# Kernel tuning notes

Measured on AMD Instinct MI355X. Metric: run time of the kernel, lower is better.

The kernel has to match this reference:

```python
import jax, jax.numpy as jnp
import numpy as np

B, K, D, R, NH, NN = 1024, 20, 128, 3, 2, 100000
DM = 3 * D          # d_model = node + edge + time feat concat
DK = DM // NH       # per-head dim
NEG = -1e10


def setup_inputs():
    key = jax.random.key(0)
    ks = jax.random.split(key, 24)
    node_table = jax.random.normal(ks[0], (NN, D), jnp.float32)
    node_table = node_table.at[0].set(0.0)  # padding_idx=0
    s = 1.0 / np.sqrt(DM)
    return {
        'src_idx': jax.random.randint(ks[1], (B,), 0, NN),
        'cut_time': jax.random.uniform(ks[2], (B,), jnp.float32) * 100.0,
        'ngh1_nodes': jax.random.randint(ks[3], (B, K), 0, NN),
        'ngh1_t': jax.random.uniform(ks[4], (B, K), jnp.float32) * 100.0,
        'ngh1_rel': jax.random.uniform(ks[5], (B, K, R), jnp.float32),
        'ngh2_nodes': jax.random.randint(ks[6], (B * K, K), 0, NN),
        'ngh2_t': jax.random.uniform(ks[7], (B * K, K), jnp.float32) * 100.0,
        'ngh2_rel': jax.random.uniform(ks[8], (B * K, K, R), jnp.float32),
        'node_table': node_table,
        'basis_freq': jnp.asarray(1.0 / np.power(10.0, np.linspace(0, 9, D)), jnp.float32),
        'phase': jnp.zeros((D,), jnp.float32),
        'rel_W': jax.random.normal(ks[9], (R, D), jnp.float32) * 0.1,
        'rel_b': jnp.zeros((D,), jnp.float32),
        'w_q': jax.random.normal(ks[10], (2, DM, DM), jnp.float32) * s,
        'w_k': jax.random.normal(ks[11], (2, DM, DM), jnp.float32) * s,
        'w_v': jax.random.normal(ks[12], (2, DM, DM), jnp.float32) * s,
        'fc_W': jax.random.normal(ks[13], (2, DM, DM), jnp.float32) * s,
        'fc_b': jnp.zeros((2, DM), jnp.float32),
        'ln_g': jnp.ones((2, DM), jnp.float32),
        'ln_b': jnp.zeros((2, DM), jnp.float32),
        'mg1_W': jax.random.normal(ks[14], (2, DM + D, D), jnp.float32) * 0.05,
        'mg1_b': jnp.zeros((2, D), jnp.float32),
        'mg2_W': jax.random.normal(ks[15], (2, D, D), jnp.float32) * 0.09,
        'mg2_b': jnp.zeros((2, D), jnp.float32),
    }


def _layer_norm(x, g, b, eps=1e-5):
    mu = x.mean(axis=-1, keepdims=True)
    var = ((x - mu) ** 2).mean(axis=-1, keepdims=True)
    return (x - mu) / jnp.sqrt(var + eps) * g + b


def _attn_agg(src, src_t, seq, seq_t, seq_e, mask,
              wq, wk, wv, fcW, fcb, g, b, m1W, m1b, m2W, m2b):
    # src [Bb,D], src_t [Bb,1,D], seq/seq_t/seq_e [Bb,N,D], mask [Bb,N] (True = pad)
    Bb, N = seq.shape[0], seq.shape[1]
    src_ext = src[:, None, :]
    q = jnp.concatenate([src_ext, jnp.zeros_like(src_ext), src_t], axis=2)  # [Bb,1,3D]
    k = jnp.concatenate([seq, seq_e, seq_t], axis=2)                        # [Bb,N,3D]
    qh = (q @ wq).reshape(Bb, 1, NH, DK)
    kh = (k @ wk).reshape(Bb, N, NH, DK)
    vh = (k @ wv).reshape(Bb, N, NH, DK)
    sc = jnp.einsum('bqhd,bkhd->bhqk', qh, kh) / jnp.sqrt(jnp.float32(DK))
    sc = jnp.where(mask[:, None, None, :], NEG, sc)
    attn = jax.nn.softmax(sc, axis=-1)
    out = jnp.einsum('bhqk,bkhd->bqhd', attn, vh).reshape(Bb, 1, DM)
    out = _layer_norm(out @ fcW + fcb + q, g, b)[:, 0]  # residual + LN, squeeze q-len
    h = jax.nn.relu(jnp.concatenate([out, src], axis=1) @ m1W + m1b)  # MergeLayer
    return h @ m2W + m2b


def reference(src_idx, cut_time, ngh1_nodes, ngh1_t, ngh1_rel,
              ngh2_nodes, ngh2_t, ngh2_rel,
              node_table, basis_freq, phase, rel_W, rel_b,
              w_q, w_k, w_v, fc_W, fc_b, ln_g, ln_b,
              mg1_W, mg1_b, mg2_W, mg2_b):
    def tenc(ts):  # TimeEncode: cos(t*w + phi), ts [..., L] -> [..., L, D]
        return jnp.cos(ts[..., None] * basis_freq + phase)

    def layer(l, src, src_t, seq, seq_t, seq_e, mask):
        return _attn_agg(src, src_t, seq, seq_t, seq_e, mask,
                         w_q[l], w_k[l], w_v[l], fc_W[l], fc_b[l],
                         ln_g[l], ln_b[l], mg1_W[l], mg1_b[l], mg2_W[l], mg2_b[l])

    feat_src = node_table[src_idx]              # [B,D]  (layer-0 conv feat)
    feat_n1 = node_table[ngh1_nodes]            # [B,K,D]
    feat_n2 = node_table[ngh2_nodes]            # [B*K,K,D]
    zt_src = tenc(jnp.zeros((B, 1), jnp.float32))      # time embed of 0 for queries
    zt_n1 = tenc(jnp.zeros((B * K, 1), jnp.float32))
    t1e = tenc(cut_time[:, None] - ngh1_t)              # [B,K,D]
    t2e = tenc(ngh1_t.reshape(-1)[:, None] - ngh2_t)    # [B*K,K,D]
    r1 = ngh1_rel @ rel_W + rel_b               # MultiHotLayer relation embed
    r2 = ngh2_rel @ rel_W + rel_b
    m1 = ngh1_nodes == 0
    m2 = ngh2_nodes == 0

    # layer 1 (attn_model_list[0]) applied to src and to flattened 1-hop neighbors
    src_l1 = layer(0, feat_src, zt_src, feat_n1, t1e, r1, m1)                      # [B,D]
    n1_l1 = layer(0, feat_n1.reshape(B * K, D), zt_n1, feat_n2, t2e, r2, m2)       # [B*K,D]
    # layer 2 (attn_model_list[1])
    out = layer(1, src_l1, zt_src, n1_l1.reshape(B, K, D), t1e, r1, m1)            # [B,D]
    return out
```

## Files before the change

### kernel.cpp

```cpp
#include <hip/hip_runtime.h>

typedef unsigned int u32;
typedef unsigned short u16;

typedef short bf16x8 __attribute__((ext_vector_type(8)));
typedef float f32x4 __attribute__((ext_vector_type(4)));

#define DD 128
#define DMM 384
#define KNB 20

__device__ __forceinline__ u16 f2b(float f){
  u32 u = __float_as_uint(f);
  u += 0x7fffu + ((u >> 16) & 1u);
  return (u16)(u >> 16);
}
__device__ __forceinline__ float b2f(u32 h){ return __uint_as_float(h << 16); }

__global__ void zt_kernel(const float* __restrict__ phase, float* __restrict__ zt){
  int d = threadIdx.x;
  if (d < DD) zt[d] = cosf(phase[d]);
}

__global__ void tcvt_kernel(const float* __restrict__ src, u16* __restrict__ dst, int K, int N){
  int i = blockIdx.x * 256 + threadIdx.x;
  if (i >= K * N) return;
  int k = i / N, n = i - k * N;
  dst[(size_t)n * K + k] = f2b(src[i]);
}

__global__ __launch_bounds__(256) void build_k_kernel(
  const float* __restrict__ node_table,
  const int*   __restrict__ nodes,
  const float* __restrict__ feat_override,
  const float* __restrict__ t_src,
  const float* __restrict__ t_ngh,
  const float* __restrict__ rel,
  const float* __restrict__ relW, const float* __restrict__ relb,
  const float* __restrict__ bfreq, const float* __restrict__ phase,
  u16* __restrict__ kmat, int nrows)
{
  int lr = blockIdx.x * 2 + (threadIdx.x >> 7);
  if (lr >= nrows) return;
  int d = threadIdx.x & 127;
  int b = lr / KNB;
  float f;
  if (feat_override) f = feat_override[(size_t)lr * DD + d];
  else { int nd = nodes[lr]; f = node_table[(size_t)nd * DD + d]; }
  float r0 = rel[(size_t)lr * 3 + 0], r1 = rel[(size_t)lr * 3 + 1], r2 = rel[(size_t)lr * 3 + 2];
  float re = r0 * relW[d] + r1 * relW[DD + d] + r2 * relW[2 * DD + d] + relb[d];
  float dt = t_src[b] - t_ngh[lr];
  float te = cosf(dt * bfreq[d] + phase[d]);
  u16* kr = kmat + (size_t)lr * DMM;
  kr[d] = f2b(f); kr[DD + d] = f2b(re); kr[2 * DD + d] = f2b(te);
}

__global__ __launch_bounds__(256) void build_q_kernel(
  const float* __restrict__ node_table,
  const int*   __restrict__ src_nodes,
  const float* __restrict__ feat_override,
  const float* __restrict__ zt,
  u16* __restrict__ qmat, float* __restrict__ srcf,
  int nb)
{
  int r = blockIdx.x * 2 + (threadIdx.x >> 7);
  if (r >= nb) return;
  int d = threadIdx.x & 127;
  float s = feat_override ? feat_override[(size_t)r * DD + d]
                          : node_table[(size_t)src_nodes[r] * DD + d];
  size_t q0 = (size_t)r * DMM;
  qmat[q0 + d] = f2b(s); qmat[q0 + DD + d] = 0; qmat[q0 + 2 * DD + d] = f2b(zt[d]);
  srcf[(size_t)r * DD + d] = s;
}

#define SAS 40
__global__ __launch_bounds__(256) void gemm_kernel(
  const u16* __restrict__ A, const u16* __restrict__ BT,
  const float* __restrict__ bias,
  float* __restrict__ Cf, u16* __restrict__ Cb,
  int M, int N, int K, int relu)
{
  __shared__ __align__(16) u16 lds[2 * 128 * SAS];
  u16* As = lds; u16* Bs = lds + 128 * SAS;
  int tid = threadIdx.x;
  int lane = tid & 63, w = tid >> 6;
  int wm = w >> 1, wn = w & 1;
  int bm = blockIdx.x, bn = blockIdx.y;
  f32x4 acc[4][4] = {};
  int r0 = tid >> 2;
  int c0 = tid & 3;
  const u16* Abase = A + (size_t)(bm * 128) * K;
  const u16* Bbase = BT + (size_t)(bn * 128) * K;
  int rr = lane & 15, kq = lane >> 4;
  for (int kt = 0; kt < K; kt += 32) {
    uint4 a0 = *(const uint4*)(Abase + (size_t)r0 * K + kt + c0 * 8);
    uint4 a1 = *(const uint4*)(Abase + (size_t)(r0 + 64) * K + kt + c0 * 8);
    uint4 b0 = *(const uint4*)(Bbase + (size_t)r0 * K + kt + c0 * 8);
    uint4 b1 = *(const uint4*)(Bbase + (size_t)(r0 + 64) * K + kt + c0 * 8);
    __syncthreads();
    *(uint4*)&As[r0 * SAS + c0 * 8] = a0;
    *(uint4*)&As[(r0 + 64) * SAS + c0 * 8] = a1;
    *(uint4*)&Bs[r0 * SAS + c0 * 8] = b0;
    *(uint4*)&Bs[(r0 + 64) * SAS + c0 * 8] = b1;
    __syncthreads();
    bf16x8 af[4], bf[4];
    #pragma unroll
    for (int i = 0; i < 4; i++) af[i] = *(const bf16x8*)&As[(wm * 64 + i * 16 + rr) * SAS + kq * 8];
    #pragma unroll
    for (int j = 0; j < 4; j++) bf[j] = *(const bf16x8*)&Bs[(wn * 64 + j * 16 + rr) * SAS + kq * 8];
    #pragma unroll
    for (int i = 0; i < 4; i++)
      #pragma unroll
      for (int j = 0; j < 4; j++)
        acc[i][j] = __builtin_amdgcn_mfma_f32_16x16x32_bf16(af[i], bf[j], acc[i][j], 0, 0, 0);
  }
  int drow = lane >> 4, dcol = lane & 15;
  #pragma unroll
  for (int i = 0; i < 4; i++) {
    #pragma unroll
    for (int j = 0; j < 4; j++) {
      int gcol = bn * 128 + wn * 64 + j * 16 + dcol;
      float bia = bias ? bias[gcol] : 0.f;
      #pragma unroll
      for (int r = 0; r < 4; r++) {
        int grow = bm * 128 + wm * 64 + i * 16 + drow * 4 + r;
        float v = acc[i][j][r] + bia;
        if (relu) v = fmaxf(v, 0.f);
        if (Cf) Cf[(size_t)grow * N + gcol] = v;
        else    Cb[(size_t)grow * N + gcol] = f2b(v);
      }
    }
  }
}

__global__ __launch_bounds__(64) void attn_kernel(
  const float* __restrict__ qh,
  const u16*  __restrict__ khvh,
  const int*  __restrict__ nodes,
  u16* __restrict__ attn_o)
{
  int b = blockIdx.x;
  int lane = threadIdx.x;
  int h = lane >> 5, t = lane & 31;
  float qv[6];
  const float* qp = qh + (size_t)b * DMM + h * 192 + t * 6;
  #pragma unroll
  for (int j = 0; j < 6; j++) qv[j] = qp[j];
  __shared__ float sc2[2][KNB];
  const float scale = 0.07216878364870323f;
  for (int n = 0; n < KNB; n++) {
    const u32* kp = (const u32*)(khvh + ((size_t)b * KNB + n) * 768 + h * 192);
    u32 u0 = kp[t * 3 + 0], u1 = kp[t * 3 + 1], u2 = kp[t * 3 + 2];
    float ps = qv[0] * b2f(u0 & 0xffffu) + qv[1] * b2f(u0 >> 16)
             + qv[2] * b2f(u1 & 0xffffu) + qv[3] * b2f(u1 >> 16)
             + qv[4] * b2f(u2 & 0xffffu) + qv[5] * b2f(u2 >> 16);
    ps += __shfl_xor(ps, 1);  ps += __shfl_xor(ps, 2);
    ps += __shfl_xor(ps, 4);  ps += __shfl_xor(ps, 8);  ps += __shfl_xor(ps, 16);
    if (t == 0) sc2[h][n] = ps * scale;
  }
  __syncthreads();
  float s[KNB]; float mx = -3.4e38f;
  #pragma unroll
  for (int n = 0; n < KNB; n++) {
    int nd = nodes[(size_t)b * KNB + n];
    float x = (nd == 0) ? -1e10f : sc2[h][n];
    s[n] = x; mx = fmaxf(mx, x);
  }
  float se = 0.f;
  #pragma unroll
  for (int n = 0; n < KNB; n++) { float e = __expf(s[n] - mx); s[n] = e; se += e; }
  float inv = 1.f / se;
  float a6[6] = {0, 0, 0, 0, 0, 0};
  for (int n = 0; n < KNB; n++) {
    float p = s[n] * inv;
    const u32* vp = (const u32*)(khvh + ((size_t)b * KNB + n) * 768 + DMM);
    u32 u0 = vp[lane * 3 + 0], u1 = vp[lane * 3 + 1], u2 = vp[lane * 3 + 2];
    a6[0] += p * b2f(u0 & 0xffffu); a6[1] += p * b2f(u0 >> 16);
    a6[2] += p * b2f(u1 & 0xffffu); a6[3] += p * b2f(u1 >> 16);
    a6[4] += p * b2f(u2 & 0xffffu); a6[5] += p * b2f(u2 >> 16);
  }
  u16* op = attn_o + (size_t)b * DMM + lane * 6;
  #pragma unroll
  for (int j = 0; j < 6; j++) op[j] = f2b(a6[j]);
}

__global__ __launch_bounds__(256) void ln_kernel(
  const float* __restrict__ fcx, const float* __restrict__ fcb,
  const float* __restrict__ srcf, const float* __restrict__ zt,
  const float* __restrict__ g, const float* __restrict__ bb,
  u16* __restrict__ cat)
{
  int r = blockIdx.x * 4 + (threadIdx.x >> 6);
  int lane = threadIdx.x & 63;
  const float* x = fcx + (size_t)r * DMM;
  float v[6]; float s = 0.f;
  #pragma unroll
  for (int j = 0; j < 6; j++) {
    int c = lane * 6 + j;
    float q = (c < DD) ? srcf[(size_t)r * DD + c] : ((c < 2 * DD) ? 0.f : zt[c - 2 * DD]);
    v[j] = x[c] + fcb[c] + q; s += v[j];
  }
  #pragma unroll
  for (int m = 1; m < 64; m <<= 1) s += __shfl_xor(s, m);
  float mu = s * (1.f / 384.f);
  float vs = 0.f;
  #pragma unroll
  for (int j = 0; j < 6; j++) { float d = v[j] - mu; vs += d * d; }
  #pragma unroll
  for (int m = 1; m < 64; m <<= 1) vs += __shfl_xor(vs, m);
  float rstd = rsqrtf(vs * (1.f / 384.f) + 1e-5f);
  u16* cr = cat + (size_t)r * (DMM + DD);
  #pragma unroll
  for (int j = 0; j < 6; j++) { int c = lane * 6 + j; cr[c] = f2b((v[j] - mu) * rstd * g[c] + bb[c]); }
  #pragma unroll
  for (int j = 0; j < 2; j++) { int c = lane * 2 + j; cr[DMM + c] = f2b(srcf[(size_t)r * DD + c]); }
}

extern "C" void kernel_launch(void* const* d_in, const int* in_sizes, int n_in,
                              void* d_out, int out_size, void* d_ws, size_t ws_size,
                              hipStream_t stream)
{
  (void)in_sizes; (void)n_in; (void)out_size;
  const int B = 1024, K = 20, D = 128, DM = 384;
  const int BKR = B * K;
  const int NC = 16, CB = BKR / NC;
  const int CM = CB * K;

  const int*   src_idx    = (const int*)  d_in[0];
  const float* cut_time   = (const float*)d_in[1];
  const int*   n1_nodes   = (const int*)  d_in[2];
  const float* n1_t       = (const float*)d_in[3];
  const float* n1_rel     = (const float*)d_in[4];
  const int*   n2_nodes   = (const int*)  d_in[5];
  const float* n2_t       = (const float*)d_in[6];
  const float* n2_rel     = (const float*)d_in[7];
  const float* node_table = (const float*)d_in[8];
  const float* bfreq      = (const float*)d_in[9];
  const float* phase      = (const float*)d_in[10];
  const float* relW       = (const float*)d_in[11];
  const float* relb       = (const float*)d_in[12];
  const float* wq         = (const float*)d_in[13];
  const float* wk         = (const float*)d_in[14];
  const float* wv         = (const float*)d_in[15];
  const float* fcW        = (const float*)d_in[16];
  const float* fcb        = (const float*)d_in[17];
  const float* lng        = (const float*)d_in[18];
  const float* lnb        = (const float*)d_in[19];
  const float* m1W        = (const float*)d_in[20];
  const float* m1b        = (const float*)d_in[21];
  const float* m2W        = (const float*)d_in[22];
  const float* m2b        = (const float*)d_in[23];

  size_t off = 0;
  auto alloc = [&](size_t bytes) -> void* {
    void* p = (char*)d_ws + off; off += (bytes + 255) & ~(size_t)255; return p;
  };
  u16*   kmat  = (u16*)  alloc((size_t)CM * DM * 2);
  u16*   khvh  = (u16*)  alloc((size_t)CM * 2 * DM * 2);
  u16*   qmat  = (u16*)  alloc((size_t)CB * DM * 2);
  float* srcf  = (float*)alloc((size_t)CB * D * 4);
  float* qh    = (float*)alloc((size_t)CB * DM * 4);
  u16*   atto  = (u16*)  alloc((size_t)CB * DM * 2);
  float* fcx   = (float*)alloc((size_t)CB * DM * 4);
  u16*   cat   = (u16*)  alloc((size_t)CB * (DM + D) * 2);
  u16*   h1    = (u16*)  alloc((size_t)CB * D * 2);
  float* n1l1  = (float*)alloc((size_t)BKR * D * 4);
  float* srcl1 = (float*)alloc((size_t)B * D * 4);
  u16*   wkvT  = (u16*)  alloc((size_t)2 * 768 * DM * 2);
  u16*   wqT   = (u16*)  alloc((size_t)2 * DM * DM * 2);
  u16*   fcWT  = (u16*)  alloc((size_t)2 * DM * DM * 2);
  u16*   m1WT  = (u16*)  alloc((size_t)2 * D * (DM + D) * 2);
  u16*   m2WT  = (u16*)  alloc((size_t)2 * D * D * 2);
  float* ztb   = (float*)alloc((size_t)D * 4);
  if (off > ws_size) return;

  zt_kernel<<<1, 128, 0, stream>>>(phase, ztb);
  auto tc = [&](const float* s, u16* dst, int Kd, int Nd) {
    int tot = Kd * Nd;
    tcvt_kernel<<<(tot + 255) / 256, 256, 0, stream>>>(s, dst, Kd, Nd);
  };
  for (int l = 0; l < 2; l++) {
    tc(wk  + (size_t)l * DM * DM, wkvT + (size_t)l * 768 * DM, DM, DM);
    tc(wv  + (size_t)l * DM * DM, wkvT + (size_t)l * 768 * DM + (size_t)DM * DM, DM, DM);
    tc(wq  + (size_t)l * DM * DM, wqT  + (size_t)l * DM * DM, DM, DM);
    tc(fcW + (size_t)l * DM * DM, fcWT + (size_t)l * DM * DM, DM, DM);
    tc(m1W + (size_t)l * (DM + D) * D, m1WT + (size_t)l * D * (DM + D), DM + D, D);
    tc(m2W + (size_t)l * D * D, m2WT + (size_t)l * D * D, D, D);
  }

  auto gemm = [&](const u16* A, const u16* Bt, const float* bias,
                  float* Cf, u16* Cb, int M, int N, int Kd, int relu) {
    dim3 g(M / 128, N / 128);
    gemm_kernel<<<g, 256, 0, stream>>>(A, Bt, bias, Cf, Cb, M, N, Kd, relu);
  };

  auto run_layer = [&](int l, const int* q_nodes, const float* q_feat, int nb,
                       const int* k_nodes, const float* k_feat,
                       const float* t_src, const float* t_ngh, const float* rel,
                       int nk, float* outp) {
    build_q_kernel<<<nb / 2, 256, 0, stream>>>(node_table, q_nodes, q_feat, ztb, qmat, srcf, nb);
    gemm(qmat, wqT + (size_t)l * DM * DM, nullptr, qh, nullptr, nb, DM, DM, 0);
    build_k_kernel<<<nk / 2, 256, 0, stream>>>(node_table, k_nodes, k_feat, t_src, t_ngh, rel,
                                               relW, relb, bfreq, phase, kmat, nk);
    gemm(kmat, wkvT + (size_t)l * 768 * DM, nullptr, nullptr, khvh, nk, 768, DM, 0);
    attn_kernel<<<nb, 64, 0, stream>>>(qh, khvh, k_nodes, atto);
    gemm(atto, fcWT + (size_t)l * DM * DM, nullptr, fcx, nullptr, nb, DM, DM, 0);
    ln_kernel<<<nb / 4, 256, 0, stream>>>(fcx, fcb + l * DM, srcf, ztb, lng + l * DM, lnb + l * DM, cat);
    gemm(cat, m1WT + (size_t)l * D * (DM + D), m1b + l * D, nullptr, h1, nb, D, DM + D, 1);
    gemm(h1, m2WT + (size_t)l * D * D, m2b + l * D, outp, nullptr, nb, D, D, 0);
  };

  run_layer(0, src_idx, nullptr, B, n1_nodes, nullptr, cut_time, n1_t, n1_rel, BKR, srcl1);

  for (int c = 0; c < NC; c++) {
    run_layer(0, n1_nodes + (size_t)c * CB, nullptr, CB,
              n2_nodes + (size_t)c * CM, nullptr,
              n1_t + (size_t)c * CB, n2_t + (size_t)c * CM, n2_rel + (size_t)c * CM * 3,
              CM, n1l1 + (size_t)c * CB * D);
  }

  run_layer(1, src_idx, srcl1, B, n1_nodes, n1l1, cut_time, n1_t, n1_rel, BKR, (float*)d_out);
}
```

Measured before the change: 2.302 ms.

## Fuse FC+LayerNorm and MLP GEMMs, fold constant query parts, use direct-to-LDS loads

The GEMM now loads tiles with global_load_lds into an XOR-swizzled LDS layout and uses a K-step of 64. The FC GEMM is fused with residual add and LayerNorm, and the two merge-MLP GEMMs are fused with the hidden activation kept in LDS. The query projection is shrunk to K=128 by precomputing the constant time-embedding contribution (qzt) and dropping the zero relation block. The Q and K build kernels are merged into one launch. These changes cut launches, intermediate global traffic and redundant FLOPs, but the fused kernels run only nb/128 blocks, which may underfill the GPU.

```diff
diff --git a/kernel.cpp b/kernel.cpp
--- a/kernel.cpp
+++ b/kernel.cpp
@@ -17,9 +17,24 @@
 }
 __device__ __forceinline__ float b2f(u32 h){ return __uint_as_float(h << 16); }
 
+__device__ __forceinline__ void gload16(const void* g, void* l){
+  __builtin_amdgcn_global_load_lds((const __attribute__((address_space(1))) void*)g,
+                                   (__attribute__((address_space(3))) void*)l, 16, 0, 0);
+}
+
 __global__ void zt_kernel(const float* __restrict__ phase, float* __restrict__ zt){
   int d = threadIdx.x;
   if (d < DD) zt[d] = cosf(phase[d]);
+}
+
+__global__ void qzt_kernel(const float* __restrict__ wq, const float* __restrict__ phase,
+                           float* __restrict__ qzt){
+  int idx = blockIdx.x * 128 + threadIdx.x;
+  int l = idx / DMM, col = idx % DMM;
+  float a = 0.f;
+  for (int d = 0; d < DD; d++)
+    a += cosf(phase[d]) * wq[(size_t)l * DMM * DMM + (size_t)(256 + d) * DMM + col];
+  qzt[idx] = a;
 }
 
 __global__ void tcvt_kernel(const float* __restrict__ src, u16* __restrict__ dst, int K, int N){
@@ -29,103 +44,91 @@
   dst[(size_t)n * K + k] = f2b(src[i]);
 }
 
-__global__ __launch_bounds__(256) void build_k_kernel(
+__global__ __launch_bounds__(256) void build_kernel(
   const float* __restrict__ node_table,
-  const int*   __restrict__ nodes,
-  const float* __restrict__ feat_override,
-  const float* __restrict__ t_src,
-  const float* __restrict__ t_ngh,
+  const int*   __restrict__ q_nodes, const float* __restrict__ q_feat,
+  const int*   __restrict__ k_nodes, const float* __restrict__ k_feat,
+  const float* __restrict__ t_src, const float* __restrict__ t_ngh,
   const float* __restrict__ rel,
   const float* __restrict__ relW, const float* __restrict__ relb,
   const float* __restrict__ bfreq, const float* __restrict__ phase,
-  u16* __restrict__ kmat, int nrows)
+  u16* __restrict__ srcb, float* __restrict__ srcf, u16* __restrict__ kmat,
+  int nb, int nk)
 {
   int lr = blockIdx.x * 2 + (threadIdx.x >> 7);
-  if (lr >= nrows) return;
   int d = threadIdx.x & 127;
-  int b = lr / KNB;
-  float f;
-  if (feat_override) f = feat_override[(size_t)lr * DD + d];
-  else { int nd = nodes[lr]; f = node_table[(size_t)nd * DD + d]; }
-  float r0 = rel[(size_t)lr * 3 + 0], r1 = rel[(size_t)lr * 3 + 1], r2 = rel[(size_t)lr * 3 + 2];
-  float re = r0 * relW[d] + r1 * relW[DD + d] + r2 * relW[2 * DD + d] + relb[d];
-  float dt = t_src[b] - t_ngh[lr];
-  float te = cosf(dt * bfreq[d] + phase[d]);
-  u16* kr = kmat + (size_t)lr * DMM;
-  kr[d] = f2b(f); kr[DD + d] = f2b(re); kr[2 * DD + d] = f2b(te);
-}
-
-__global__ __launch_bounds__(256) void build_q_kernel(
-  const float* __restrict__ node_table,
-  const int*   __restrict__ src_nodes,
-  const float* __restrict__ feat_override,
-  const float* __restrict__ zt,
-  u16* __restrict__ qmat, float* __restrict__ srcf,
-  int nb)
-{
-  int r = blockIdx.x * 2 + (threadIdx.x >> 7);
-  if (r >= nb) return;
-  int d = threadIdx.x & 127;
-  float s = feat_override ? feat_override[(size_t)r * DD + d]
-                          : node_table[(size_t)src_nodes[r] * DD + d];
-  size_t q0 = (size_t)r * DMM;
-  qmat[q0 + d] = f2b(s); qmat[q0 + DD + d] = 0; qmat[q0 + 2 * DD + d] = f2b(zt[d]);
-  srcf[(size_t)r * DD + d] = s;
-}
-
-#define SAS 40
+  if (lr < nb) {
+    float s = q_feat ? q_feat[(size_t)lr * DD + d]
+                     : node_table[(size_t)q_nodes[lr] * DD + d];
+    srcb[(size_t)lr * DD + d] = f2b(s);
+    srcf[(size_t)lr * DD + d] = s;
+  } else {
+    int r = lr - nb;
+    if (r >= nk) return;
+    int b = r / KNB;
+    float f;
+    if (k_feat) f = k_feat[(size_t)r * DD + d];
+    else { int nd = k_nodes[r]; f = node_table[(size_t)nd * DD + d]; }
+    float r0 = rel[(size_t)r * 3 + 0], r1 = rel[(size_t)r * 3 + 1], r2 = rel[(size_t)r * 3 + 2];
+    float re = r0 * relW[d] + r1 * relW[DD + d] + r2 * relW[2 * DD + d] + relb[d];
+    float dt = t_src[b] - t_ngh[r];
+    float te = cosf(dt * bfreq[d] + phase[d]);
+    u16* kr = kmat + (size_t)r * DMM;
+    kr[d] = f2b(f); kr[DD + d] = f2b(re); kr[2 * DD + d] = f2b(te);
+  }
+}
+
 __global__ __launch_bounds__(256) void gemm_kernel(
   const u16* __restrict__ A, const u16* __restrict__ BT,
   const float* __restrict__ bias,
   float* __restrict__ Cf, u16* __restrict__ Cb,
-  int M, int N, int K, int relu)
+  int N, int K)
 {
-  __shared__ __align__(16) u16 lds[2 * 128 * SAS];
-  u16* As = lds; u16* Bs = lds + 128 * SAS;
-  int tid = threadIdx.x;
-  int lane = tid & 63, w = tid >> 6;
+  __shared__ __align__(16) u16 As[128 * 64];
+  __shared__ __align__(16) u16 Bs[128 * 64];
+  int tid = threadIdx.x, lane = tid & 63, w = tid >> 6;
   int wm = w >> 1, wn = w & 1;
-  int bm = blockIdx.x, bn = blockIdx.y;
+  int rr = lane & 15, kq = lane >> 4;
+  int crow = lane >> 3;
+  int sslot = (lane & 7) ^ crow;
+  const u16* Ab = A + (size_t)(blockIdx.x * 128) * K;
+  const u16* Bb = BT + (size_t)(blockIdx.y * 128) * K;
   f32x4 acc[4][4] = {};
-  int r0 = tid >> 2;
-  int c0 = tid & 3;
-  const u16* Abase = A + (size_t)(bm * 128) * K;
-  const u16* Bbase = BT + (size_t)(bn * 128) * K;
-  int rr = lane & 15, kq = lane >> 4;
-  for (int kt = 0; kt < K; kt += 32) {
-    uint4 a0 = *(const uint4*)(Abase + (size_t)r0 * K + kt + c0 * 8);
-    uint4 a1 = *(const uint4*)(Abase + (size_t)(r0 + 64) * K + kt + c0 * 8);
-    uint4 b0 = *(const uint4*)(Bbase + (size_t)r0 * K + kt + c0 * 8);
-    uint4 b1 = *(const uint4*)(Bbase + (size_t)(r0 + 64) * K + kt + c0 * 8);
-    __syncthreads();
-    *(uint4*)&As[r0 * SAS + c0 * 8] = a0;
-    *(uint4*)&As[(r0 + 64) * SAS + c0 * 8] = a1;
-    *(uint4*)&Bs[r0 * SAS + c0 * 8] = b0;
-    *(uint4*)&Bs[(r0 + 64) * SAS + c0 * 8] = b1;
-    __syncthreads();
-    bf16x8 af[4], bf[4];
-    #pragma unroll
-    for (int i = 0; i < 4; i++) af[i] = *(const bf16x8*)&As[(wm * 64 + i * 16 + rr) * SAS + kq * 8];
-    #pragma unroll
-    for (int j = 0; j < 4; j++) bf[j] = *(const bf16x8*)&Bs[(wn * 64 + j * 16 + rr) * SAS + kq * 8];
-    #pragma unroll
-    for (int i = 0; i < 4; i++)
-      #pragma unroll
-      for (int j = 0; j < 4; j++)
-        acc[i][j] = __builtin_amdgcn_mfma_f32_16x16x32_bf16(af[i], bf[j], acc[i][j], 0, 0, 0);
+  for (int kt = 0; kt < K; kt += 64) {
+    __syncthreads();
+    #pragma unroll
+    for (int cc = 0; cc < 4; cc++) {
+      int c = w * 4 + cc;
+      gload16(Ab + (size_t)(c * 8 + crow) * K + kt + sslot * 8, &As[c * 512]);
+      gload16(Bb + (size_t)(c * 8 + crow) * K + kt + sslot * 8, &Bs[c * 512]);
+    }
+    __syncthreads();
+    #pragma unroll
+    for (int ks = 0; ks < 2; ks++) {
+      int spb = (ks * 4 + kq) ^ (rr & 7);
+      bf16x8 af[4], bf[4];
+      #pragma unroll
+      for (int i = 0; i < 4; i++) af[i] = *(const bf16x8*)&As[(wm * 64 + i * 16 + rr) * 64 + spb * 8];
+      #pragma unroll
+      for (int j = 0; j < 4; j++) bf[j] = *(const bf16x8*)&Bs[(wn * 64 + j * 16 + rr) * 64 + spb * 8];
+      #pragma unroll
+      for (int i = 0; i < 4; i++)
+        #pragma unroll
+        for (int j = 0; j < 4; j++)
+          acc[i][j] = __builtin_amdgcn_mfma_f32_16x16x32_bf16(af[i], bf[j], acc[i][j], 0, 0, 0);
+    }
   }
   int drow = lane >> 4, dcol = lane & 15;
   #pragma unroll
   for (int i = 0; i < 4; i++) {
     #pragma unroll
     for (int j = 0; j < 4; j++) {
-      int gcol = bn * 128 + wn * 64 + j * 16 + dcol;
+      int gcol = blockIdx.y * 128 + wn * 64 + j * 16 + dcol;
       float bia = bias ? bias[gcol] : 0.f;
       #pragma unroll
       for (int r = 0; r < 4; r++) {
-        int grow = bm * 128 + wm * 64 + i * 16 + drow * 4 + r;
+        int grow = blockIdx.x * 128 + wm * 64 + i * 16 + drow * 4 + r;
         float v = acc[i][j][r] + bia;
-        if (relu) v = fmaxf(v, 0.f);
         if (Cf) Cf[(size_t)grow * N + gcol] = v;
         else    Cb[(size_t)grow * N + gcol] = f2b(v);
       }
@@ -184,36 +187,232 @@
   for (int j = 0; j < 6; j++) op[j] = f2b(a6[j]);
 }
 
-__global__ __launch_bounds__(256) void ln_kernel(
-  const float* __restrict__ fcx, const float* __restrict__ fcb,
-  const float* __restrict__ srcf, const float* __restrict__ zt,
-  const float* __restrict__ g, const float* __restrict__ bb,
-  u16* __restrict__ cat)
+__global__ __launch_bounds__(512) void fcln_kernel(
+  const u16* __restrict__ atto, const u16* __restrict__ fcWT,
+  const float* __restrict__ fcb, const float* __restrict__ srcf,
+  const float* __restrict__ zt, const float* __restrict__ g,
+  const float* __restrict__ bb, u16* __restrict__ cat)
 {
-  int r = blockIdx.x * 4 + (threadIdx.x >> 6);
-  int lane = threadIdx.x & 63;
-  const float* x = fcx + (size_t)r * DMM;
-  float v[6]; float s = 0.f;
-  #pragma unroll
-  for (int j = 0; j < 6; j++) {
-    int c = lane * 6 + j;
-    float q = (c < DD) ? srcf[(size_t)r * DD + c] : ((c < 2 * DD) ? 0.f : zt[c - 2 * DD]);
-    v[j] = x[c] + fcb[c] + q; s += v[j];
-  }
-  #pragma unroll
-  for (int m = 1; m < 64; m <<= 1) s += __shfl_xor(s, m);
-  float mu = s * (1.f / 384.f);
-  float vs = 0.f;
-  #pragma unroll
-  for (int j = 0; j < 6; j++) { float d = v[j] - mu; vs += d * d; }
-  #pragma unroll
-  for (int m = 1; m < 64; m <<= 1) vs += __shfl_xor(vs, m);
-  float rstd = rsqrtf(vs * (1.f / 384.f) + 1e-5f);
-  u16* cr = cat + (size_t)r * (DMM + DD);
-  #pragma unroll
-  for (int j = 0; j < 6; j++) { int c = lane * 6 + j; cr[c] = f2b((v[j] - mu) * rstd * g[c] + bb[c]); }
-  #pragma unroll
-  for (int j = 0; j < 2; j++) { int c = lane * 2 + j; cr[DMM + c] = f2b(srcf[(size_t)r * DD + c]); }
+  __shared__ __align__(16) u16 As[128 * 64];
+  __shared__ __align__(16) u16 Bs[384 * 64];
+  __shared__ float rsum[128][4];
+  int tid = threadIdx.x, lane = tid & 63, w = tid >> 6;
+  int wm = w >> 2, wn = w & 3;
+  int rr = lane & 15, kq = lane >> 4;
+  int crow = lane >> 3, sslot = (lane & 7) ^ crow;
+  int row0 = blockIdx.x * 128;
+  const u16* Ab = atto + (size_t)row0 * DMM;
+  f32x4 acc[4][6] = {};
+  for (int kt = 0; kt < DMM; kt += 64) {
+    __syncthreads();
+    #pragma unroll
+    for (int cc = 0; cc < 2; cc++) {
+      int c = w * 2 + cc;
+      gload16(Ab + (size_t)(c * 8 + crow) * DMM + kt + sslot * 8, &As[c * 512]);
+    }
+    #pragma unroll
+    for (int cc = 0; cc < 6; cc++) {
+      int c = w * 6 + cc;
+      gload16(fcWT + (size_t)(c * 8 + crow) * DMM + kt + sslot * 8, &Bs[c * 512]);
+    }
+    __syncthreads();
+    #pragma unroll
+    for (int ks = 0; ks < 2; ks++) {
+      int spb = (ks * 4 + kq) ^ (rr & 7);
+      bf16x8 af[4], bf[6];
+      #pragma unroll
+      for (int i = 0; i < 4; i++) af[i] = *(const bf16x8*)&As[(wm * 64 + i * 16 + rr) * 64 + spb * 8];
+      #pragma unroll
+      for (int j = 0; j < 6; j++) bf[j] = *(const bf16x8*)&Bs[(wn * 96 + j * 16 + rr) * 64 + spb * 8];
+      #pragma unroll
+      for (int i = 0; i < 4; i++)
+        #pragma unroll
+        for (int j = 0; j < 6; j++)
+          acc[i][j] = __builtin_amdgcn_mfma_f32_16x16x32_bf16(af[i], bf[j], acc[i][j], 0, 0, 0);
+    }
+  }
+  int drow = lane >> 4, dcol = lane & 15;
+  #pragma unroll
+  for (int i = 0; i < 4; i++) {
+    #pragma unroll
+    for (int j = 0; j < 6; j++) {
+      int col = wn * 96 + j * 16 + dcol;
+      float fb = fcb[col] + ((col >= 2 * DD) ? zt[col - 2 * DD] : 0.f);
+      #pragma unroll
+      for (int r = 0; r < 4; r++) {
+        int row = row0 + wm * 64 + i * 16 + drow * 4 + r;
+        float qv = (col < DD) ? srcf[(size_t)row * DD + col] : 0.f;
+        acc[i][j][r] += fb + qv;
+      }
+    }
+  }
+  float pr[4][4];
+  #pragma unroll
+  for (int i = 0; i < 4; i++)
+    #pragma unroll
+    for (int r = 0; r < 4; r++) {
+      float s = 0.f;
+      #pragma unroll
+      for (int j = 0; j < 6; j++) s += acc[i][j][r];
+      #pragma unroll
+      for (int m = 1; m < 16; m <<= 1) s += __shfl_xor(s, m);
+      pr[i][r] = s;
+    }
+  if ((lane & 15) == 0) {
+    #pragma unroll
+    for (int i = 0; i < 4; i++)
+      #pragma unroll
+      for (int r = 0; r < 4; r++)
+        rsum[wm * 64 + i * 16 + drow * 4 + r][wn] = pr[i][r];
+  }
+  __syncthreads();
+  float mu[4][4];
+  #pragma unroll
+  for (int i = 0; i < 4; i++)
+    #pragma unroll
+    for (int r = 0; r < 4; r++) {
+      int R = wm * 64 + i * 16 + drow * 4 + r;
+      mu[i][r] = (rsum[R][0] + rsum[R][1] + rsum[R][2] + rsum[R][3]) * (1.f / 384.f);
+    }
+  __syncthreads();
+  #pragma unroll
+  for (int i = 0; i < 4; i++)
+    #pragma unroll
+    for (int r = 0; r < 4; r++) {
+      float s = 0.f;
+      #pragma unroll
+      for (int j = 0; j < 6; j++) { float d = acc[i][j][r] - mu[i][r]; s += d * d; }
+      #pragma unroll
+      for (int m = 1; m < 16; m <<= 1) s += __shfl_xor(s, m);
+      pr[i][r] = s;
+    }
+  if ((lane & 15) == 0) {
+    #pragma unroll
+    for (int i = 0; i < 4; i++)
+      #pragma unroll
+      for (int r = 0; r < 4; r++)
+        rsum[wm * 64 + i * 16 + drow * 4 + r][wn] = pr[i][r];
+  }
+  __syncthreads();
+  float rstd[4][4];
+  #pragma unroll
+  for (int i = 0; i < 4; i++)
+    #pragma unroll
+    for (int r = 0; r < 4; r++) {
+      int R = wm * 64 + i * 16 + drow * 4 + r;
+      float vv = (rsum[R][0] + rsum[R][1] + rsum[R][2] + rsum[R][3]) * (1.f / 384.f);
+      rstd[i][r] = rsqrtf(vv + 1e-5f);
+    }
+  #pragma unroll
+  for (int i = 0; i < 4; i++)
+    #pragma unroll
+    for (int j = 0; j < 6; j++) {
+      int col = wn * 96 + j * 16 + dcol;
+      float gg = g[col], bbb = bb[col];
+      #pragma unroll
+      for (int r = 0; r < 4; r++) {
+        int row = row0 + wm * 64 + i * 16 + drow * 4 + r;
+        float val = (acc[i][j][r] - mu[i][r]) * rstd[i][r] * gg + bbb;
+        cat[(size_t)row * 512 + col] = f2b(val);
+      }
+    }
+  for (int e = tid; e < 128 * DD; e += 512) {
+    int r2 = e >> 7, c2 = e & 127;
+    cat[(size_t)(row0 + r2) * 512 + DMM + c2] = f2b(srcf[(size_t)(row0 + r2) * DD + c2]);
+  }
+}
+
+__global__ __launch_bounds__(256) void mg_kernel(
+  const u16* __restrict__ cat, const u16* __restrict__ m1WT, const float* __restrict__ m1b,
+  const u16* __restrict__ m2WT, const float* __restrict__ m2b,
+  float* __restrict__ out)
+{
+  __shared__ __align__(16) u16 As[128 * 64];
+  __shared__ __align__(16) u16 Bs[128 * 64];
+  __shared__ __align__(16) u16 Hs[128 * 128];
+  int tid = threadIdx.x, lane = tid & 63, w = tid >> 6;
+  int wm = w >> 1, wn = w & 1;
+  int rr = lane & 15, kq = lane >> 4;
+  int crow = lane >> 3, sslot = (lane & 7) ^ crow;
+  int row0 = blockIdx.x * 128;
+  const u16* Ab = cat + (size_t)row0 * 512;
+  f32x4 acc[4][4] = {};
+  for (int kt = 0; kt < 512; kt += 64) {
+    __syncthreads();
+    #pragma unroll
+    for (int cc = 0; cc < 4; cc++) {
+      int c = w * 4 + cc;
+      gload16(Ab + (size_t)(c * 8 + crow) * 512 + kt + sslot * 8, &As[c * 512]);
+      gload16(m1WT + (size_t)(c * 8 + crow) * 512 + kt + sslot * 8, &Bs[c * 512]);
+    }
+    __syncthreads();
+    #pragma unroll
+    for (int ks = 0; ks < 2; ks++) {
+      int spb = (ks * 4 + kq) ^ (rr & 7);
+      bf16x8 af[4], bf[4];
+      #pragma unroll
+      for (int i = 0; i < 4; i++) af[i] = *(const bf16x8*)&As[(wm * 64 + i * 16 + rr) * 64 + spb * 8];
+      #pragma unroll
+      for (int j = 0; j < 4; j++) bf[j] = *(const bf16x8*)&Bs[(wn * 64 + j * 16 + rr) * 64 + spb * 8];
+      #pragma unroll
+      for (int i = 0; i < 4; i++)
+        #pragma unroll
+        for (int j = 0; j < 4; j++)
+          acc[i][j] = __builtin_amdgcn_mfma_f32_16x16x32_bf16(af[i], bf[j], acc[i][j], 0, 0, 0);
+    }
+  }
+  int drow = lane >> 4, dcol = lane & 15;
+  __syncthreads();
+  #pragma unroll
+  for (int i = 0; i < 4; i++)
+    #pragma unroll
+    for (int j = 0; j < 4; j++) {
+      int col = wn * 64 + j * 16 + dcol;
+      float mb = m1b[col];
+      #pragma unroll
+      for (int r = 0; r < 4; r++) {
+        int row = wm * 64 + i * 16 + drow * 4 + r;
+        float v = fmaxf(acc[i][j][r] + mb, 0.f);
+        Hs[row * 128 + (((col >> 3) ^ (row & 7)) << 3) + (col & 7)] = f2b(v);
+      }
+    }
+  f32x4 acc2[4][4] = {};
+  for (int kt = 0; kt < 128; kt += 64) {
+    #pragma unroll
+    for (int cc = 0; cc < 4; cc++) {
+      int c = w * 4 + cc;
+      gload16(m2WT + (size_t)(c * 8 + crow) * 128 + kt + sslot * 8, &Bs[c * 512]);
+    }
+    __syncthreads();
+    #pragma unroll
+    for (int ks = 0; ks < 2; ks++) {
+      int spb = (ks * 4 + kq) ^ (rr & 7);
+      int slh = ((kt >> 3) + ks * 4 + kq) ^ (rr & 7);
+      bf16x8 af[4], bf[4];
+      #pragma unroll
+      for (int i = 0; i < 4; i++) af[i] = *(const bf16x8*)&Hs[(wm * 64 + i * 16 + rr) * 128 + slh * 8];
+      #pragma unroll
+      for (int j = 0; j < 4; j++) bf[j] = *(const bf16x8*)&Bs[(wn * 64 + j * 16 + rr) * 64 + spb * 8];
+      #pragma unroll
+      for (int i = 0; i < 4; i++)
+        #pragma unroll
+        for (int j = 0; j < 4; j++)
+          acc2[i][j] = __builtin_amdgcn_mfma_f32_16x16x32_bf16(af[i], bf[j], acc2[i][j], 0, 0, 0);
+    }
+    __syncthreads();
+  }
+  #pragma unroll
+  for (int i = 0; i < 4; i++)
+    #pragma unroll
+    for (int j = 0; j < 4; j++) {
+      int col = wn * 64 + j * 16 + dcol;
+      float mb = m2b[col];
+      #pragma unroll
+      for (int r = 0; r < 4; r++) {
+        int row = row0 + wm * 64 + i * 16 + drow * 4 + r;
+        out[(size_t)row * DD + col] = acc2[i][j][r] + mb;
+      }
+    }
 }
 
 extern "C" void kernel_launch(void* const* d_in, const int* in_sizes, int n_in,
@@ -257,24 +456,24 @@
   };
   u16*   kmat  = (u16*)  alloc((size_t)CM * DM * 2);
   u16*   khvh  = (u16*)  alloc((size_t)CM * 2 * DM * 2);
-  u16*   qmat  = (u16*)  alloc((size_t)CB * DM * 2);
+  u16*   srcb  = (u16*)  alloc((size_t)CB * D * 2);
   float* srcf  = (float*)alloc((size_t)CB * D * 4);
   float* qh    = (float*)alloc((size_t)CB * DM * 4);
   u16*   atto  = (u16*)  alloc((size_t)CB * DM * 2);
-  float* fcx   = (float*)alloc((size_t)CB * DM * 4);
   u16*   cat   = (u16*)  alloc((size_t)CB * (DM + D) * 2);
-  u16*   h1    = (u16*)  alloc((size_t)CB * D * 2);
   float* n1l1  = (float*)alloc((size_t)BKR * D * 4);
   float* srcl1 = (float*)alloc((size_t)B * D * 4);
   u16*   wkvT  = (u16*)  alloc((size_t)2 * 768 * DM * 2);
-  u16*   wqT   = (u16*)  alloc((size_t)2 * DM * DM * 2);
+  u16*   wqTT  = (u16*)  alloc((size_t)2 * DM * D * 2);
   u16*   fcWT  = (u16*)  alloc((size_t)2 * DM * DM * 2);
   u16*   m1WT  = (u16*)  alloc((size_t)2 * D * (DM + D) * 2);
   u16*   m2WT  = (u16*)  alloc((size_t)2 * D * D * 2);
+  float* qzt   = (float*)alloc((size_t)2 * DM * 4);
   float* ztb   = (float*)alloc((size_t)D * 4);
   if (off > ws_size) return;
 
   zt_kernel<<<1, 128, 0, stream>>>(phase, ztb);
+  qzt_kernel<<<6, 128, 0, stream>>>(wq, phase, qzt);
   auto tc = [&](const float* s, u16* dst, int Kd, int Nd) {
     int tot = Kd * Nd;
     tcvt_kernel<<<(tot + 255) / 256, 256, 0, stream>>>(s, dst, Kd, Nd);
@@ -282,32 +481,36 @@
   for (int l = 0; l < 2; l++) {
     tc(wk  + (size_t)l * DM * DM, wkvT + (size_t)l * 768 * DM, DM, DM);
     tc(wv  + (size_t)l * DM * DM, wkvT + (size_t)l * 768 * DM + (size_t)DM * DM, DM, DM);
-    tc(wq  + (size_t)l * DM * DM, wqT  + (size_t)l * DM * DM, DM, DM);
+    tc(wq  + (size_t)l * DM * DM, wqTT + (size_t)l * DM * D, D, DM);
     tc(fcW + (size_t)l * DM * DM, fcWT + (size_t)l * DM * DM, DM, DM);
     tc(m1W + (size_t)l * (DM + D) * D, m1WT + (size_t)l * D * (DM + D), DM + D, D);
     tc(m2W + (size_t)l * D * D, m2WT + (size_t)l * D * D, D, D);
   }
-
-  auto gemm = [&](const u16* A, const u16* Bt, const float* bias,
-                  float* Cf, u16* Cb, int M, int N, int Kd, int relu) {
-    dim3 g(M / 128, N / 128);
-    gemm_kernel<<<g, 256, 0, stream>>>(A, Bt, bias, Cf, Cb, M, N, Kd, relu);
-  };
 
   auto run_layer = [&](int l, const int* q_nodes, const float* q_feat, int nb,
                        const int* k_nodes, const float* k_feat,
                        const float* t_src, const float* t_ngh, const float* rel,
                        int nk, float* outp) {
-    build_q_kernel<<<nb / 2, 256, 0, stream>>>(node_table, q_nodes, q_feat, ztb, qmat, srcf, nb);
-    gemm(qmat, wqT + (size_t)l * DM * DM, nullptr, qh, nullptr, nb, DM, DM, 0);
-    build_k_kernel<<<nk / 2, 256, 0, stream>>>(node_table, k_nodes, k_feat, t_src, t_ngh, rel,
-                                               relW, relb, bfreq, phase, kmat, nk);
-    gemm(kmat, wkvT + (size_t)l * 768 * DM, nullptr, nullptr, khvh, nk, 768, DM, 0);
+    build_kernel<<<(nb + nk) / 2, 256, 0, stream>>>(
+        node_table, q_nodes, q_feat, k_nodes, k_feat, t_src, t_ngh, rel,
+        relW, relb, bfreq, phase, srcb, srcf, kmat, nb, nk);
+    {
+      dim3 g(nb / 128, 3);
+      gemm_kernel<<<g, 256, 0, stream>>>(srcb, wqTT + (size_t)l * DM * D,
+                                         qzt + (size_t)l * DM, qh, nullptr, DM, D);
+    }
+    {
+      dim3 g(nk / 128, 6);
+      gemm_kernel<<<g, 256, 0, stream>>>(kmat, wkvT + (size_t)l * 768 * DM,
+                                         nullptr, nullptr, khvh, 768, DM);
+    }
     attn_kernel<<<nb, 64, 0, stream>>>(qh, khvh, k_nodes, atto);
-    gemm(atto, fcWT + (size_t)l * DM * DM, nullptr, fcx, nullptr, nb, DM, DM, 0);
-    ln_kernel<<<nb / 4, 256, 0, stream>>>(fcx, fcb + l * DM, srcf, ztb, lng + l * DM, lnb + l * DM, cat);
-    gemm(cat, m1WT + (size_t)l * D * (DM + D), m1b + l * D, nullptr, h1, nb, D, DM + D, 1);
-    gemm(h1, m2WT + (size_t)l * D * D, m2b + l * D, outp, nullptr, nb, D, D, 0);
+    fcln_kernel<<<nb / 128, 512, 0, stream>>>(atto, fcWT + (size_t)l * DM * DM,
+                                              fcb + l * DM, srcf, ztb,
+                                              lng + l * DM, lnb + l * DM, cat);
+    mg_kernel<<<nb / 128, 256, 0, stream>>>(cat, m1WT + (size_t)l * D * (DM + D),
+                                            m1b + l * D, m2WT + (size_t)l * D * D,
+                                            m2b + l * D, outp);
   };
 
   run_layer(0, src_idx, nullptr, B, n1_nodes, nullptr, cut_time, n1_t, n1_rel, BKR, srcl1);
```

After: 1.891 ms. -17.9%, faster.
